# Kernel optimization log

Hardware: AMD Instinct MI355X
Metric: run time of the kernel (lower is better)

The kernel has to match this reference:

```python
import jax, jax.numpy as jnp
import numpy as np

NUDGE = 1e-7

def _norm(x):
    # global mean + L2-norm over axes (1,2), per sample (faithful to source)
    size = x.shape[1] * x.shape[2]
    mean = jnp.sum(x, axis=(1, 2), keepdims=True) / size
    xc = x - mean
    l2 = jnp.sqrt(jnp.sum(xc * xc, axis=(1, 2), keepdims=True))
    return xc / (l2 + NUDGE)


def setup_inputs() -> dict:
    key = jax.random.key(0)
    ks = jax.random.split(key, 9)
    B, D, S, F = 8, 512, 4096, 2048
    s = 0.02
    x = jax.random.normal(ks[0], (B, D, S), dtype=jnp.float32)
    Wq = jax.random.normal(ks[1], (D, D), dtype=jnp.float32) * s
    Wk = jax.random.normal(ks[2], (D, D), dtype=jnp.float32) * s
    Wv = jax.random.normal(ks[3], (D, D), dtype=jnp.float32) * s
    Wo = jax.random.normal(ks[4], (D, D), dtype=jnp.float32) * s
    W1 = jax.random.normal(ks[5], (D, F), dtype=jnp.float32) * s
    b1 = jnp.zeros((F,), dtype=jnp.float32)
    W2 = jax.random.normal(ks[6], (F, D), dtype=jnp.float32) * s
    b2 = jnp.zeros((D,), dtype=jnp.float32)
    return {"x": x, "Wq": Wq, "Wk": Wk, "Wv": Wv, "Wo": Wo,
            "W1": W1, "b1": b1, "W2": W2, "b2": b2}


def reference(x, Wq, Wk, Wv, Wo, W1, b1, W2, b2):
    B, D, S = x.shape
    xt = jnp.swapaxes(x, 1, 2)                      # [B,S,D]
    q = xt @ Wq                                     # [B,S,D]
    k = xt @ Wk
    v = xt @ Wv
    scores = jnp.einsum('bsd,btd->bst', q, k) / jnp.sqrt(jnp.float32(D))
    attn = jax.nn.softmax(scores, axis=-1)          # [B,S,S]
    attn_out = jnp.swapaxes((attn @ v) @ Wo, 1, 2)  # [B,D,S]

    post = _norm(x + attn_out)                      # [B,D,S]

    # per-slice feedforward+linear loop == batched matmul over token axis
    pt = jnp.swapaxes(post, 1, 2)                   # [B,S,D]
    h = jax.nn.relu(pt @ W1 + b1) @ W2 + b2         # [B,S,D]
    return _norm(post + jnp.swapaxes(h, 1, 2))
```

## Files before the change

### kernel.cpp

```cpp
#include <hip/hip_runtime.h>


typedef unsigned short u16;
typedef __attribute__((ext_vector_type(4))) float f32x4;
typedef __attribute__((ext_vector_type(8))) short s16x8;

__device__ __forceinline__ float bf2f(u16 u) {
    unsigned int v = ((unsigned int)u) << 16;
    float f;
    __builtin_memcpy(&f, &v, 4);
    return f;
}
__device__ __forceinline__ u16 f2bf(float f) {
    unsigned int v;
    __builtin_memcpy(&v, &f, 4);
    unsigned int r = (v + 0x7fffu + ((v >> 16) & 1u)) >> 16;
    return (u16)r;
}
__device__ __forceinline__ u16 loadbf(const void* p, long long i, int f32) {
    return f32 ? f2bf(((const float*)p)[i]) : ((const u16*)p)[i];
}

#if defined(__has_builtin)
#if __has_builtin(__builtin_amdgcn_global_load_lds)
#define HAS_GLDS 1
#endif
#endif
#ifndef HAS_GLDS
#define HAS_GLDS 0
#endif

#if HAS_GLDS
__device__ __forceinline__ void glds16(const u16* g, u16* l) {
    __builtin_amdgcn_global_load_lds(
        (const __attribute__((address_space(1))) void*)g,
        (__attribute__((address_space(3))) void*)l, 16, 0, 0);
}
#endif

__global__ __launch_bounds__(256) void detect_f32(
    const u16* __restrict__ p, int n_u16, int* __restrict__ flag)
{
    int insane = 0;
    for (int i = threadIdx.x; i < n_u16; i += 256) {
        u16 h = p[i];
        int e = (h >> 7) & 0xFF;
        int m = h & 0x7F;
        bool sane = (e >= 96 && e <= 141) || (e == 0 && m == 0);
        insane += sane ? 0 : 1;
    }
#pragma unroll
    for (int off = 32; off > 0; off >>= 1) insane += __shfl_down(insane, off);
    __shared__ int red[4];
    if ((threadIdx.x & 63) == 0) red[threadIdx.x >> 6] = insane;
    __syncthreads();
    if (threadIdx.x == 0)
        *flag = (red[0] + red[1] + red[2] + red[3] > n_u16 / 4) ? 1 : 0;
}

#define BM 128
#define BN 128
#define BK 32

template <typename OutT, bool BIAS, bool RELU, bool EXPSUM, bool RDIV>
__global__ __launch_bounds__(256) void gemm_bt(
    const u16* __restrict__ A, const u16* __restrict__ Bt, OutT* __restrict__ C,
    const u16* __restrict__ bias, int M, int N, int K,
    int lda, int ldb, int ldc, int wmod,
    long long aZ, long long aW, long long bZ, long long bW, long long cZ,
    int swz, float* rs, long long rsZ)
{
    __shared__ u16 As[2][BM * BK];
    __shared__ u16 Bs[2][BN * BK];

    const int z = blockIdx.z;
    const int g = z / wmod, w = z - g * wmod;
    A  += g * aZ + w * aW;
    Bt += g * bZ + w * bW;
    C  += (long long)z * cZ;
    if (EXPSUM || RDIV) rs += z * rsZ;

    int bx = blockIdx.x, by = blockIdx.y;
    if (swz) {
        const int gx = gridDim.x;
        int id = by * gx + bx;
        int xcd = id & 7, j = id >> 3;
        bx = j % gx;
        by = (j / gx) * 8 + xcd;
    }

    const int tid = threadIdx.x;
    const int wave = tid >> 6, lane = tid & 63;
    const int wm = wave >> 1, wn = wave & 1;
    const int q = lane >> 4, r = lane & 15;

    const int ar = tid >> 2;
    const int ac = (((tid & 3) ^ ((tid >> 3) & 3)) << 3);
    const int ks = (r >> 1) & 3;

    const u16* Ag = A + (long long)(by * BM + ar) * lda + ac;
    const u16* Bg = Bt + (long long)(bx * BN + ar) * ldb + ac;
    const long long rstepA = 64LL * lda, rstepB = 64LL * ldb;

    f32x4 acc[4][4];
    const f32x4 zero = {0.f, 0.f, 0.f, 0.f};
#pragma unroll
    for (int i = 0; i < 4; ++i)
#pragma unroll
        for (int j = 0; j < 4; ++j) acc[i][j] = zero;

    const int nIter = K / BK;
#if HAS_GLDS
    glds16(Ag, &As[0][tid * 8]);
    glds16(Ag + rstepA, &As[0][2048 + tid * 8]);
    glds16(Bg, &Bs[0][tid * 8]);
    glds16(Bg + rstepB, &Bs[0][2048 + tid * 8]);
    Ag += BK; Bg += BK;
    __syncthreads();
    for (int it = 0; it < nIter; ++it) {
        const int cur = it & 1, nxt = cur ^ 1;
        if (it + 1 < nIter) {
            glds16(Ag, &As[nxt][tid * 8]);
            glds16(Ag + rstepA, &As[nxt][2048 + tid * 8]);
            glds16(Bg, &Bs[nxt][tid * 8]);
            glds16(Bg + rstepB, &Bs[nxt][2048 + tid * 8]);
            Ag += BK; Bg += BK;
        }
        s16x8 af[4], bf[4];
#pragma unroll
        for (int mi = 0; mi < 4; ++mi)
            af[mi] = *(const s16x8*)(&As[cur][(wm * 64 + mi * 16 + r) * BK + ((q ^ ks) << 3)]);
#pragma unroll
        for (int ni = 0; ni < 4; ++ni)
            bf[ni] = *(const s16x8*)(&Bs[cur][(wn * 64 + ni * 16 + r) * BK + ((q ^ ks) << 3)]);
#pragma unroll
        for (int mi = 0; mi < 4; ++mi)
#pragma unroll
            for (int ni = 0; ni < 4; ++ni)
                acc[mi][ni] = __builtin_amdgcn_mfma_f32_16x16x32_bf16(
                    af[mi], bf[ni], acc[mi][ni], 0, 0, 0);
        __syncthreads();
    }
#else
    for (int it = 0; it < nIter; ++it) {
        int4 a0 = *(const int4*)(Ag);
        int4 a1 = *(const int4*)(Ag + rstepA);
        int4 b0 = *(const int4*)(Bg);
        int4 b1 = *(const int4*)(Bg + rstepB);
        Ag += BK; Bg += BK;
        __syncthreads();
        *(int4*)(&As[0][tid * 8]) = a0;
        *(int4*)(&As[0][2048 + tid * 8]) = a1;
        *(int4*)(&Bs[0][tid * 8]) = b0;
        *(int4*)(&Bs[0][2048 + tid * 8]) = b1;
        __syncthreads();
        s16x8 af[4], bf[4];
#pragma unroll
        for (int mi = 0; mi < 4; ++mi)
            af[mi] = *(const s16x8*)(&As[0][(wm * 64 + mi * 16 + r) * BK + ((q ^ ks) << 3)]);
#pragma unroll
        for (int ni = 0; ni < 4; ++ni)
            bf[ni] = *(const s16x8*)(&Bs[0][(wn * 64 + ni * 16 + r) * BK + ((q ^ ks) << 3)]);
#pragma unroll
        for (int mi = 0; mi < 4; ++mi)
#pragma unroll
            for (int ni = 0; ni < 4; ++ni)
                acc[mi][ni] = __builtin_amdgcn_mfma_f32_16x16x32_bf16(
                    af[mi], bf[ni], acc[mi][ni], 0, 0, 0);
    }
#endif

    const int col0 = bx * BN + wn * 64;
    const int row0 = by * BM + wm * 64;
    if constexpr (EXPSUM) {
        const float scale = 0.044194173824159216f;
#pragma unroll
        for (int mi = 0; mi < 4; ++mi) {
#pragma unroll
            for (int rr = 0; rr < 4; ++rr) {
                const int rowg = row0 + mi * 16 + q * 4 + rr;
                float rsum = 0.f;
#pragma unroll
                for (int ni = 0; ni < 4; ++ni) {
                    float v = __expf(fminf(acc[mi][ni][rr] * scale, 30.f));
                    rsum += v;
                    C[(long long)rowg * ldc + col0 + ni * 16 + r] = (OutT)f2bf(v);
                }
#pragma unroll
                for (int o = 1; o < 16; o <<= 1) rsum += __shfl_xor(rsum, o);
                if (r == 0) atomicAdd(&rs[rowg], rsum);
            }
        }
    } else {
#pragma unroll
        for (int ni = 0; ni < 4; ++ni) {
            const int colg = col0 + ni * 16 + r;
            float bv = 0.f;
            if constexpr (BIAS) bv = bf2f(bias[colg]);
#pragma unroll
            for (int mi = 0; mi < 4; ++mi) {
#pragma unroll
                for (int rr = 0; rr < 4; ++rr) {
                    const int rowg = row0 + mi * 16 + q * 4 + rr;
                    float v = acc[mi][ni][rr] + bv;
                    if constexpr (RELU) v = fmaxf(v, 0.f);
                    if constexpr (RDIV) v /= rs[rowg];
                    if constexpr (sizeof(OutT) == 2)
                        C[(long long)rowg * ldc + colg] = (OutT)f2bf(v);
                    else
                        C[(long long)rowg * ldc + colg] = (OutT)v;
                }
            }
        }
    }
}

__global__ __launch_bounds__(256) void transpose_any(
    const void* __restrict__ in, u16* __restrict__ out, int R, int C,
    long long sIn, long long sOut, const int* __restrict__ flag)
{
    __shared__ u16 tile[32][33];
    const int f32 = *flag;
    const long long ib = (long long)blockIdx.z * sIn;
    u16* ob = out + (long long)blockIdx.z * sOut;
    const int c0 = blockIdx.x * 32, r0 = blockIdx.y * 32;
    const int tx = threadIdx.x, ty = threadIdx.y;
#pragma unroll
    for (int i = 0; i < 4; ++i) {
        int rr = ty + i * 8;
        tile[rr][tx] = loadbf(in, ib + (long long)(r0 + rr) * C + c0 + tx, f32);
    }
    __syncthreads();
#pragma unroll
    for (int i = 0; i < 4; ++i) {
        int cc = ty + i * 8;
        ob[(long long)(c0 + cc) * R + r0 + tx] = tile[tx][cc];
    }
}

__global__ __launch_bounds__(256) void transpose_b16(
    const u16* __restrict__ in, u16* __restrict__ out, int R, int C,
    long long sIn, long long sOut)
{
    __shared__ u16 tile[32][33];
    in += (long long)blockIdx.z * sIn;
    out += (long long)blockIdx.z * sOut;
    const int c0 = blockIdx.x * 32, r0 = blockIdx.y * 32;
    const int tx = threadIdx.x, ty = threadIdx.y;
#pragma unroll
    for (int i = 0; i < 4; ++i) {
        int rr = ty + i * 8;
        tile[rr][tx] = in[(long long)(r0 + rr) * C + c0 + tx];
    }
    __syncthreads();
#pragma unroll
    for (int i = 0; i < 4; ++i) {
        int cc = ty + i * 8;
        out[(long long)(c0 + cc) * R + r0 + tx] = tile[tx][cc];
    }
}

__global__ __launch_bounds__(256) void convert_bias(
    const void* __restrict__ b1, const void* __restrict__ b2,
    u16* __restrict__ ob, const int* __restrict__ f1, const int* __restrict__ f2)
{
    int i = blockIdx.x * 256 + threadIdx.x;
    if (i < 2048) ob[i] = loadbf(b1, i, *f1);
    else if (i < 2560) ob[i] = loadbf(b2, i - 2048, *f2);
}

__global__ __launch_bounds__(256) void reduce_legs(
    const float* __restrict__ P, u16* __restrict__ O, int legs,
    const float* __restrict__ l)
{
    const long long SD = 4096LL * 512;
    const int g = blockIdx.y;
    const float* Pg = P + (long long)g * legs * SD;
    const float* lg = l + (long long)g * 4096;
    u16* Og = O + (long long)g * SD;
    const int base = blockIdx.x * 2048;
#pragma unroll
    for (int it = 0; it < 8; ++it) {
        int i = base + it * 256 + threadIdx.x;
        float s = 0.f;
        for (int lj = 0; lj < legs; ++lj) s += Pg[(long long)lj * SD + i];
        Og[i] = f2bf(s / lg[i >> 9]);
    }
}

__global__ __launch_bounds__(256) void stats_add_partial(
    const u16* __restrict__ A, const u16* __restrict__ Bv,
    float2* __restrict__ partial)
{
    const int b = blockIdx.y;
    const long long yb = (long long)b * (4096LL * 512);
    const int base = blockIdx.x * 2048;
    float s = 0.f, ss = 0.f;
#pragma unroll
    for (int it = 0; it < 8; ++it) {
        int i = base + it * 256 + threadIdx.x;
        float z = bf2f(A[yb + i]) + bf2f(Bv[yb + i]);
        s += z; ss += z * z;
    }
#pragma unroll
    for (int off = 32; off > 0; off >>= 1) {
        s += __shfl_down(s, off); ss += __shfl_down(ss, off);
    }
    __shared__ float red[8];
    int lane = threadIdx.x & 63, wave = threadIdx.x >> 6;
    if (lane == 0) { red[wave * 2] = s; red[wave * 2 + 1] = ss; }
    __syncthreads();
    if (threadIdx.x == 0) {
        for (int w = 1; w < 4; ++w) { s += red[w * 2]; ss += red[w * 2 + 1]; }
        partial[b * 1024 + blockIdx.x] = make_float2(s, ss);
    }
}

__global__ __launch_bounds__(256) void stats_finish(
    const float2* __restrict__ partial, float2* __restrict__ stats, float N)
{
    const int b = blockIdx.x;
    float s = 0.f, ss = 0.f;
    for (int i = threadIdx.x; i < 1024; i += 256) {
        float2 p = partial[b * 1024 + i];
        s += p.x; ss += p.y;
    }
#pragma unroll
    for (int off = 32; off > 0; off >>= 1) {
        s += __shfl_down(s, off); ss += __shfl_down(ss, off);
    }
    __shared__ float red[8];
    int lane = threadIdx.x & 63, wave = threadIdx.x >> 6;
    if (lane == 0) { red[wave * 2] = s; red[wave * 2 + 1] = ss; }
    __syncthreads();
    if (threadIdx.x == 0) {
        for (int w = 1; w < 4; ++w) { s += red[w * 2]; ss += red[w * 2 + 1]; }
        float mean = s / N;
        float l2 = sqrtf(fmaxf(ss - s * s / N, 0.f));
        stats[b] = make_float2(mean, 1.f / (l2 + 1e-7f));
    }
}

__global__ __launch_bounds__(256) void post_kernel(
    const u16* __restrict__ A, const u16* __restrict__ Bv,
    const float2* __restrict__ stats, u16* __restrict__ post)
{
    const int b = blockIdx.y;
    const float2 st = stats[b];
    const long long yb = (long long)b * (4096LL * 512);
    const int base = blockIdx.x * 2048;
#pragma unroll
    for (int it = 0; it < 8; ++it) {
        int i = base + it * 256 + threadIdx.x;
        float z = bf2f(A[yb + i]) + bf2f(Bv[yb + i]);
        post[yb + i] = f2bf((z - st.x) * st.y);
    }
}

__global__ __launch_bounds__(256) void final_kernel(
    const u16* __restrict__ P, const u16* __restrict__ G,
    const float2* __restrict__ stats, float* __restrict__ out)
{
    __shared__ float tile[32][33];
    const int b = blockIdx.z;
    const float2 st = stats[b];
    const long long bb = (long long)b * (4096LL * 512);
    const int s0 = blockIdx.x * 32, d0 = blockIdx.y * 32;
    const int tx = threadIdx.x, ty = threadIdx.y;
#pragma unroll
    for (int i = 0; i < 4; ++i) {
        int sl = ty + i * 8;
        long long idx = bb + (long long)(s0 + sl) * 512 + d0 + tx;
        tile[sl][tx] = bf2f(P[idx]) + bf2f(G[idx]);
    }
    __syncthreads();
#pragma unroll
    for (int i = 0; i < 4; ++i) {
        int dl = ty + i * 8;
        out[bb + (long long)(d0 + dl) * 4096 + s0 + tx] =
            (tile[tx][dl] - st.x) * st.y;
    }
}

extern "C" void kernel_launch(void* const* d_in, const int* in_sizes, int n_in,
                              void* d_out, int out_size, void* d_ws, size_t ws_size,
                              hipStream_t stream)
{
    (void)out_size;
    const void* x  = d_in[0];
    const void* Wq = d_in[1];
    const void* Wk = d_in[2];
    const void* Wv = d_in[3];
    const void* Wo = d_in[4];
    const void* W1 = d_in[5];
    const void* b1 = d_in[6];
    const void* W2 = d_in[7];
    const void* b2 = d_in[8];

    const int Bb = 8, D = 512, S = 4096, F = 2048;
    const long long SD = (long long)S * D;
    const long long DD = (long long)D * D;
    const long long SS = (long long)S * S;

    char* ws = (char*)d_ws;
    size_t off = 0;
    auto take = [&](size_t bytes) -> char* {
        char* p = ws + off;
        off += (bytes + 255) & ~(size_t)255;
        return p;
    };
    u16* xt   = (u16*)take((size_t)Bb * SD * 2);
    u16* WqT  = (u16*)take((size_t)DD * 2);
    u16* WkT  = (u16*)take((size_t)DD * 2);
    u16* WvT  = (u16*)take((size_t)DD * 2);
    u16* WoT  = (u16*)take((size_t)DD * 2);
    u16* W1T  = (u16*)take((size_t)D * F * 2);
    u16* W2T  = (u16*)take((size_t)D * F * 2);
    u16* bb   = (u16*)take(2560 * 2);
    u16* post = (u16*)take((size_t)Bb * SD * 2);
    float2* npart  = (float2*)take(8 * 1024 * sizeof(float2));
    float2* stats1v = (float2*)take(256);
    float2* stats2v = (float2*)take(256);
    int* flags = (int*)take(16 * sizeof(int));
    float* rowsums = (float*)take((size_t)Bb * S * sizeof(float));

    size_t remaining = ws_size > off ? ws_size - off : 0;
    const size_t perG = (size_t)4 * SD * 2 + (size_t)SS * 2 + 65536;
    int G = (remaining >= 8 * perG) ? 8 : (remaining >= 4 * perG) ? 4
          : (remaining >= 2 * perG) ? 2 : 1;
    int legs = (G == 1) ? 4 : (G == 2) ? 2 : 1;

    u16* QKV    = (u16*)take((size_t)3 * G * SD * 2);
    u16* Vt     = (u16*)take((size_t)G * SD * 2);
    u16* scores = (u16*)take((size_t)G * SS * 2);
    float* partK = (float*)post;
    u16* Oall = (u16*)d_out;
    u16* Y    = scores;
    u16* Hbuf = (u16*)d_out;
    u16* Gbuf = scores;

    for (int i = 0; i < 9 && i < n_in; ++i) {
        int n = in_sizes[i] < 8192 ? in_sizes[i] : 8192;
        detect_f32<<<1, 256, 0, stream>>>((const u16*)d_in[i], n, flags + i);
    }

    dim3 tb(32, 8, 1);
    transpose_any<<<dim3(S / 32, D / 32, Bb), tb, 0, stream>>>(x, xt, D, S, SD, SD, flags + 0);
    transpose_any<<<dim3(16, 16, 1), tb, 0, stream>>>(Wq, WqT, D, D, 0, 0, flags + 1);
    transpose_any<<<dim3(16, 16, 1), tb, 0, stream>>>(Wk, WkT, D, D, 0, 0, flags + 2);
    transpose_any<<<dim3(16, 16, 1), tb, 0, stream>>>(Wv, WvT, D, D, 0, 0, flags + 3);
    transpose_any<<<dim3(16, 16, 1), tb, 0, stream>>>(Wo, WoT, D, D, 0, 0, flags + 4);
    transpose_any<<<dim3(F / 32, D / 32, 1), tb, 0, stream>>>(W1, W1T, D, F, 0, 0, flags + 5);
    transpose_any<<<dim3(D / 32, F / 32, 1), tb, 0, stream>>>(W2, W2T, F, D, 0, 0, flags + 7);
    convert_bias<<<10, 256, 0, stream>>>(b1, b2, bb, flags + 6, flags + 8);
    hipMemsetAsync(rowsums, 0, (size_t)Bb * S * sizeof(float), stream);

    for (int b0 = 0; b0 < Bb; b0 += G) {
        gemm_bt<u16, false, false, false, false><<<dim3(D / 128, S / 128, 3 * G), 256, 0, stream>>>(
            xt + (long long)b0 * SD, WqT, QKV, nullptr, S, D, D, D, D, D,
            3, SD, 0, 0, DD, SD, 1, nullptr, 0);
        transpose_b16<<<dim3(D / 32, S / 32, G), tb, 0, stream>>>(
            QKV + 2 * SD, Vt, S, D, 3 * SD, SD);
        gemm_bt<u16, false, false, true, false><<<dim3(S / 128, S / 128, G), 256, 0, stream>>>(
            QKV, QKV + SD, scores, nullptr, S, S, D, D, D, S,
            1, 3 * SD, 0, 3 * SD, 0, SS, 1, rowsums + (long long)b0 * S, S);
        if (legs == 1) {
            gemm_bt<u16, false, false, false, true><<<dim3(D / 128, S / 128, G), 256, 0, stream>>>(
                scores, Vt, Oall + (long long)b0 * SD, nullptr, S, D, S, S, S, D,
                1, SS, 0, SD, 0, SD, 1, rowsums + (long long)b0 * S, S);
        } else {
            gemm_bt<float, false, false, false, false><<<dim3(D / 128, S / 128, G * legs), 256, 0, stream>>>(
                scores, Vt, partK, nullptr, S, D, S / legs, S, S, D,
                legs, SS, S / legs, SD, S / legs, SD, 1, nullptr, 0);
            reduce_legs<<<dim3(1024, G), 256, 0, stream>>>(
                partK, Oall + (long long)b0 * SD, legs, rowsums + (long long)b0 * S);
        }
    }

    gemm_bt<u16, false, false, false, false><<<dim3(D / 128, (Bb * S) / 128, 1), 256, 0, stream>>>(
        Oall, WoT, Y, nullptr, Bb * S, D, D, D, D, D, 1, 0, 0, 0, 0, 0, 1, nullptr, 0);

    stats_add_partial<<<dim3(1024, Bb), 256, 0, stream>>>(xt, Y, npart);
    stats_finish<<<dim3(Bb), 256, 0, stream>>>(npart, stats1v, (float)SD);
    post_kernel<<<dim3(1024, Bb), 256, 0, stream>>>(xt, Y, stats1v, post);

    for (int h = 0; h < 2; ++h) {
        gemm_bt<u16, true, true, false, false><<<dim3(F / 128, (4 * S) / 128, 1), 256, 0, stream>>>(
            post + (long long)h * 4 * SD, W1T, Hbuf, bb, 4 * S, F, D, D, D, F,
            1, 0, 0, 0, 0, 0, 1, nullptr, 0);
        gemm_bt<u16, true, false, false, false><<<dim3(D / 128, (4 * S) / 128, 1), 256, 0, stream>>>(
            Hbuf, W2T, Gbuf + (long long)h * 4 * SD, bb + 2048, 4 * S, D, F, F, F, D,
            1, 0, 0, 0, 0, 0, 1, nullptr, 0);
    }

    stats_add_partial<<<dim3(1024, Bb), 256, 0, stream>>>(post, Gbuf, npart);
    stats_finish<<<dim3(Bb), 256, 0, stream>>>(npart, stats2v, (float)SD);
    final_kernel<<<dim3(S / 32, D / 32, Bb), tb, 0, stream>>>(
        post, Gbuf, stats2v, (float*)d_out);
}
```

Before: 1.148 ms.

## Fuse attention into flash-style kernel and batch input dtype detection

Replaces the separate QK^T exp-score GEMM plus PV GEMM, which wrote a full SxS score matrix to memory, with a fused flash-attention kernel. It keeps Q tiles in LDS, streams K tiles, forms exp-probabilities in LDS and accumulates P·V in registers, then normalizes by the row sums. The max-free exp with clamp is kept, and an optional split-K path with a reduction kernel remains for small workspaces. The nine per-input detect launches are merged into one kernel. The new kernel uses large LDS and 512 threads, so occupancy is low, and V is read directly from global memory without staging.

```diff
diff --git a/kernel.cpp b/kernel.cpp
--- a/kernel.cpp
+++ b/kernel.cpp
@@ -36,11 +36,18 @@
         (const __attribute__((address_space(1))) void*)g,
         (__attribute__((address_space(3))) void*)l, 16, 0, 0);
 }
+#else
+__device__ __forceinline__ void glds16(const u16* g, u16* l) {
+    *(int4*)l = *(const int4*)g;
+}
 #endif
 
-__global__ __launch_bounds__(256) void detect_f32(
-    const u16* __restrict__ p, int n_u16, int* __restrict__ flag)
-{
+struct DetectArgs { const u16* p[9]; int n[9]; };
+
+__global__ __launch_bounds__(256) void detect9(DetectArgs a, int* __restrict__ flags)
+{
+    const u16* p = a.p[blockIdx.x];
+    const int n_u16 = a.n[blockIdx.x];
     int insane = 0;
     for (int i = threadIdx.x; i < n_u16; i += 256) {
         u16 h = p[i];
@@ -55,20 +62,20 @@
     if ((threadIdx.x & 63) == 0) red[threadIdx.x >> 6] = insane;
     __syncthreads();
     if (threadIdx.x == 0)
-        *flag = (red[0] + red[1] + red[2] + red[3] > n_u16 / 4) ? 1 : 0;
+        flags[blockIdx.x] = (red[0] + red[1] + red[2] + red[3] > n_u16 / 4) ? 1 : 0;
 }
 
 #define BM 128
 #define BN 128
 #define BK 32
 
-template <typename OutT, bool BIAS, bool RELU, bool EXPSUM, bool RDIV>
+template <typename OutT, bool BIAS, bool RELU>
 __global__ __launch_bounds__(256) void gemm_bt(
     const u16* __restrict__ A, const u16* __restrict__ Bt, OutT* __restrict__ C,
     const u16* __restrict__ bias, int M, int N, int K,
     int lda, int ldb, int ldc, int wmod,
     long long aZ, long long aW, long long bZ, long long bW, long long cZ,
-    int swz, float* rs, long long rsZ)
+    int swz)
 {
     __shared__ u16 As[2][BM * BK];
     __shared__ u16 Bs[2][BN * BK];
@@ -78,7 +85,6 @@
     A  += g * aZ + w * aW;
     Bt += g * bZ + w * bW;
     C  += (long long)z * cZ;
-    if (EXPSUM || RDIV) rs += z * rsZ;
 
     int bx = blockIdx.x, by = blockIdx.y;
     if (swz) {
@@ -110,7 +116,6 @@
         for (int j = 0; j < 4; ++j) acc[i][j] = zero;
 
     const int nIter = K / BK;
-#if HAS_GLDS
     glds16(Ag, &As[0][tid * 8]);
     glds16(Ag + rstepA, &As[0][2048 + tid * 8]);
     glds16(Bg, &Bs[0][tid * 8]);
@@ -141,77 +146,239 @@
                     af[mi], bf[ni], acc[mi][ni], 0, 0, 0);
         __syncthreads();
     }
-#else
-    for (int it = 0; it < nIter; ++it) {
-        int4 a0 = *(const int4*)(Ag);
-        int4 a1 = *(const int4*)(Ag + rstepA);
-        int4 b0 = *(const int4*)(Bg);
-        int4 b1 = *(const int4*)(Bg + rstepB);
-        Ag += BK; Bg += BK;
-        __syncthreads();
-        *(int4*)(&As[0][tid * 8]) = a0;
-        *(int4*)(&As[0][2048 + tid * 8]) = a1;
-        *(int4*)(&Bs[0][tid * 8]) = b0;
-        *(int4*)(&Bs[0][2048 + tid * 8]) = b1;
-        __syncthreads();
-        s16x8 af[4], bf[4];
-#pragma unroll
-        for (int mi = 0; mi < 4; ++mi)
-            af[mi] = *(const s16x8*)(&As[0][(wm * 64 + mi * 16 + r) * BK + ((q ^ ks) << 3)]);
-#pragma unroll
-        for (int ni = 0; ni < 4; ++ni)
-            bf[ni] = *(const s16x8*)(&Bs[0][(wn * 64 + ni * 16 + r) * BK + ((q ^ ks) << 3)]);
-#pragma unroll
-        for (int mi = 0; mi < 4; ++mi)
-#pragma unroll
-            for (int ni = 0; ni < 4; ++ni)
-                acc[mi][ni] = __builtin_amdgcn_mfma_f32_16x16x32_bf16(
-                    af[mi], bf[ni], acc[mi][ni], 0, 0, 0);
-    }
-#endif
 
     const int col0 = bx * BN + wn * 64;
     const int row0 = by * BM + wm * 64;
-    if constexpr (EXPSUM) {
-        const float scale = 0.044194173824159216f;
+#pragma unroll
+    for (int ni = 0; ni < 4; ++ni) {
+        const int colg = col0 + ni * 16 + r;
+        float bv = 0.f;
+        if constexpr (BIAS) bv = bf2f(bias[colg]);
 #pragma unroll
         for (int mi = 0; mi < 4; ++mi) {
 #pragma unroll
             for (int rr = 0; rr < 4; ++rr) {
                 const int rowg = row0 + mi * 16 + q * 4 + rr;
-                float rsum = 0.f;
-#pragma unroll
-                for (int ni = 0; ni < 4; ++ni) {
-                    float v = __expf(fminf(acc[mi][ni][rr] * scale, 30.f));
-                    rsum += v;
-                    C[(long long)rowg * ldc + col0 + ni * 16 + r] = (OutT)f2bf(v);
+                float v = acc[mi][ni][rr] + bv;
+                if constexpr (RELU) v = fmaxf(v, 0.f);
+                if constexpr (sizeof(OutT) == 2)
+                    C[(long long)rowg * ldc + colg] = (OutT)f2bf(v);
+                else
+                    C[(long long)rowg * ldc + colg] = (OutT)v;
+            }
+        }
+    }
+}
+
+template <bool DIRECT>
+__global__ __launch_bounds__(512, 2) void flash_attn(
+    const u16* __restrict__ QKV,
+    const u16* __restrict__ Vt,
+    u16* __restrict__ O,
+    float* __restrict__ Opart,
+    float* __restrict__ rsPart,
+    int nsplit)
+{
+    __shared__ u16 Qs[64 * 512];
+    __shared__ u16 Ks[2][128 * 128];
+    __shared__ u16 Ps[64 * 136];
+    __shared__ float rsL[8][64];
+
+    const long long SD = 4096LL * 512;
+    const int g = blockIdx.z, sp = blockIdx.y;
+    const int q0 = blockIdx.x * 64;
+    const u16* Qg = QKV + ((long long)g * 3 + 0) * SD;
+    const u16* Kg = QKV + ((long long)g * 3 + 1) * SD;
+    const u16* Vg = Vt + (long long)g * SD;
+
+    const int tid = threadIdx.x;
+    const int wave = tid >> 6, lane = tid & 63;
+    const int q = lane >> 4, r = lane & 15;
+    const int mg = wave >> 2, ng = wave & 3;
+    const int dg = wave;
+
+#pragma unroll
+    for (int i = 0; i < 8; ++i) {
+        int L = i * 512 + tid;
+        int row = L >> 6, p = L & 63;
+        int l = p ^ (row & 15);
+        glds16(Qg + (long long)(q0 + row) * 512 + l * 8, &Qs[L * 8]);
+    }
+
+    f32x4 oacc[4][4];
+    const f32x4 zero = {0.f, 0.f, 0.f, 0.f};
+#pragma unroll
+    for (int i = 0; i < 4; ++i)
+#pragma unroll
+        for (int j = 0; j < 4; ++j) oacc[i][j] = zero;
+    float rsum[2][4] = {{0.f, 0.f, 0.f, 0.f}, {0.f, 0.f, 0.f, 0.f}};
+
+    const int span = 4096 / nsplit;
+    const int kt0 = sp * span;
+    const int ktN = span / 128;
+    const float scale = 0.044194173824159216f;
+
+    auto stageK = [&](int ktile, int kc, int buf) {
+#pragma unroll
+        for (int i = 0; i < 4; ++i) {
+            int L = i * 512 + tid;
+            int row = L >> 4, p = L & 15;
+            int l = p ^ (row & 15);
+            glds16(Kg + (long long)(kt0 + ktile * 128 + row) * 512 + kc * 128 + l * 8,
+                   &Ks[buf][L * 8]);
+        }
+    };
+    stageK(0, 0, 0);
+
+    for (int kt = 0; kt < ktN; ++kt) {
+        f32x4 sacc[2][2];
+#pragma unroll
+        for (int i = 0; i < 2; ++i)
+#pragma unroll
+            for (int j = 0; j < 2; ++j) sacc[i][j] = zero;
+
+        for (int kc = 0; kc < 4; ++kc) {
+            if (kc < 3) stageK(kt, kc + 1, (kc + 1) & 1);
+            __syncthreads();
+            const u16* Kb = Ks[kc & 1];
+#pragma unroll
+            for (int sc = 0; sc < 4; ++sc) {
+                s16x8 af[2], bf[2];
+#pragma unroll
+                for (int mi = 0; mi < 2; ++mi) {
+                    int row = (mg * 2 + mi) * 16 + r;
+                    int l = kc * 16 + sc * 4 + q;
+                    af[mi] = *(const s16x8*)&Qs[row * 512 + ((l ^ r) << 3)];
                 }
 #pragma unroll
-                for (int o = 1; o < 16; o <<= 1) rsum += __shfl_xor(rsum, o);
-                if (r == 0) atomicAdd(&rs[rowg], rsum);
+                for (int ni = 0; ni < 2; ++ni) {
+                    int row = (ng * 2 + ni) * 16 + r;
+                    int l = sc * 4 + q;
+                    bf[ni] = *(const s16x8*)&Kb[row * 128 + ((l ^ r) << 3)];
+                }
+#pragma unroll
+                for (int mi = 0; mi < 2; ++mi)
+#pragma unroll
+                    for (int ni = 0; ni < 2; ++ni)
+                        sacc[mi][ni] = __builtin_amdgcn_mfma_f32_16x16x32_bf16(
+                            af[mi], bf[ni], sacc[mi][ni], 0, 0, 0);
             }
         }
-    } else {
-#pragma unroll
-        for (int ni = 0; ni < 4; ++ni) {
-            const int colg = col0 + ni * 16 + r;
-            float bv = 0.f;
-            if constexpr (BIAS) bv = bf2f(bias[colg]);
-#pragma unroll
-            for (int mi = 0; mi < 4; ++mi) {
+#pragma unroll
+        for (int mi = 0; mi < 2; ++mi) {
+#pragma unroll
+            for (int ni = 0; ni < 2; ++ni) {
+                int col = (ng * 2 + ni) * 16 + r;
 #pragma unroll
                 for (int rr = 0; rr < 4; ++rr) {
-                    const int rowg = row0 + mi * 16 + q * 4 + rr;
-                    float v = acc[mi][ni][rr] + bv;
-                    if constexpr (RELU) v = fmaxf(v, 0.f);
-                    if constexpr (RDIV) v /= rs[rowg];
-                    if constexpr (sizeof(OutT) == 2)
-                        C[(long long)rowg * ldc + colg] = (OutT)f2bf(v);
-                    else
-                        C[(long long)rowg * ldc + colg] = (OutT)v;
+                    int row = (mg * 2 + mi) * 16 + q * 4 + rr;
+                    float v = __expf(fminf(sacc[mi][ni][rr] * scale, 30.f));
+                    Ps[row * 136 + col] = f2bf(v);
+                    rsum[mi][rr] += v;
                 }
             }
         }
+        if (kt + 1 < ktN) stageK(kt + 1, 0, 0);
+        __syncthreads();
+        const long long vbase = (long long)(dg * 64 + r) * 4096 + kt0 + kt * 128;
+#pragma unroll
+        for (int kc = 0; kc < 4; ++kc) {
+            s16x8 af[4], bf[4];
+#pragma unroll
+            for (int mi = 0; mi < 4; ++mi)
+                af[mi] = *(const s16x8*)(Vg + vbase + (long long)mi * 16 * 4096
+                                         + kc * 32 + q * 8);
+#pragma unroll
+            for (int ni = 0; ni < 4; ++ni)
+                bf[ni] = *(const s16x8*)&Ps[(ni * 16 + r) * 136 + kc * 32 + q * 8];
+#pragma unroll
+            for (int mi = 0; mi < 4; ++mi)
+#pragma unroll
+                for (int ni = 0; ni < 4; ++ni)
+                    oacc[mi][ni] = __builtin_amdgcn_mfma_f32_16x16x32_bf16(
+                        af[mi], bf[ni], oacc[mi][ni], 0, 0, 0);
+        }
+    }
+
+#pragma unroll
+    for (int mi = 0; mi < 2; ++mi)
+#pragma unroll
+        for (int rr = 0; rr < 4; ++rr) {
+            float s = rsum[mi][rr];
+#pragma unroll
+            for (int m = 1; m < 16; m <<= 1) s += __shfl_xor(s, m);
+            rsum[mi][rr] = s;
+        }
+    if (r == 0) {
+#pragma unroll
+        for (int mi = 0; mi < 2; ++mi)
+#pragma unroll
+            for (int rr = 0; rr < 4; ++rr)
+                rsL[wave][(mg * 2 + mi) * 16 + q * 4 + rr] = rsum[mi][rr];
+    }
+    __syncthreads();
+
+    if constexpr (DIRECT) {
+        u16* Og = O + (long long)g * SD;
+#pragma unroll
+        for (int ni = 0; ni < 4; ++ni) {
+            int qrow = ni * 16 + r;
+            int wb = (qrow >> 5) * 4;
+            float rs = rsL[wb][qrow] + rsL[wb + 1][qrow]
+                     + rsL[wb + 2][qrow] + rsL[wb + 3][qrow];
+            float inv = 1.f / rs;
+#pragma unroll
+            for (int mi = 0; mi < 4; ++mi) {
+                int d = (dg * 4 + mi) * 16 + q * 4;
+                ushort4 o4;
+                o4.x = f2bf(oacc[mi][ni][0] * inv);
+                o4.y = f2bf(oacc[mi][ni][1] * inv);
+                o4.z = f2bf(oacc[mi][ni][2] * inv);
+                o4.w = f2bf(oacc[mi][ni][3] * inv);
+                *(ushort4*)&Og[(long long)(q0 + qrow) * 512 + d] = o4;
+            }
+        }
+    } else {
+        const int pb = g * nsplit + sp;
+        float* Op = Opart + (long long)pb * SD;
+#pragma unroll
+        for (int ni = 0; ni < 4; ++ni) {
+            int qrow = ni * 16 + r;
+#pragma unroll
+            for (int mi = 0; mi < 4; ++mi) {
+                int d = (dg * 4 + mi) * 16 + q * 4;
+                float4 o4;
+                o4.x = oacc[mi][ni][0]; o4.y = oacc[mi][ni][1];
+                o4.z = oacc[mi][ni][2]; o4.w = oacc[mi][ni][3];
+                *(float4*)&Op[(long long)(q0 + qrow) * 512 + d] = o4;
+            }
+        }
+        if (tid < 64) {
+            int wb = (tid >> 5) * 4;
+            rsPart[(long long)pb * 4096 + q0 + tid] =
+                rsL[wb][tid] + rsL[wb + 1][tid] + rsL[wb + 2][tid] + rsL[wb + 3][tid];
+        }
+    }
+}
+
+__global__ __launch_bounds__(256) void reduce_flash(
+    const float* __restrict__ Opart, const float* __restrict__ rsPart,
+    u16* __restrict__ O, int ns)
+{
+    const long long SD = 4096LL * 512;
+    const int g = blockIdx.y;
+    u16* Og = O + (long long)g * SD;
+    const int base = blockIdx.x * 2048;
+#pragma unroll
+    for (int it = 0; it < 8; ++it) {
+        int i = base + it * 256 + threadIdx.x;
+        int row = i >> 9;
+        float s = 0.f, rs = 0.f;
+        for (int sp = 0; sp < ns; ++sp) {
+            s += Opart[(long long)(g * ns + sp) * SD + i];
+            rs += rsPart[(long long)(g * ns + sp) * 4096 + row];
+        }
+        Og[i] = f2bf(s / rs);
     }
 }
 
@@ -267,25 +434,6 @@
     int i = blockIdx.x * 256 + threadIdx.x;
     if (i < 2048) ob[i] = loadbf(b1, i, *f1);
     else if (i < 2560) ob[i] = loadbf(b2, i - 2048, *f2);
-}
-
-__global__ __launch_bounds__(256) void reduce_legs(
-    const float* __restrict__ P, u16* __restrict__ O, int legs,
-    const float* __restrict__ l)
-{
-    const long long SD = 4096LL * 512;
-    const int g = blockIdx.y;
-    const float* Pg = P + (long long)g * legs * SD;
-    const float* lg = l + (long long)g * 4096;
-    u16* Og = O + (long long)g * SD;
-    const int base = blockIdx.x * 2048;
-#pragma unroll
-    for (int it = 0; it < 8; ++it) {
-        int i = base + it * 256 + threadIdx.x;
-        float s = 0.f;
-        for (int lj = 0; lj < legs; ++lj) s += Pg[(long long)lj * SD + i];
-        Og[i] = f2bf(s / lg[i >> 9]);
-    }
 }
 
 __global__ __launch_bounds__(256) void stats_add_partial(
@@ -400,7 +548,6 @@
     const int Bb = 8, D = 512, S = 4096, F = 2048;
     const long long SD = (long long)S * D;
     const long long DD = (long long)D * D;
-    const long long SS = (long long)S * S;
 
     char* ws = (char*)d_ws;
     size_t off = 0;
@@ -422,27 +569,28 @@
     float2* stats1v = (float2*)take(256);
     float2* stats2v = (float2*)take(256);
     int* flags = (int*)take(16 * sizeof(int));
-    float* rowsums = (float*)take((size_t)Bb * S * sizeof(float));
+    float* rsPart = (float*)take(4 * 4096 * sizeof(float));
 
     size_t remaining = ws_size > off ? ws_size - off : 0;
-    const size_t perG = (size_t)4 * SD * 2 + (size_t)SS * 2 + 65536;
-    int G = (remaining >= 8 * perG) ? 8 : (remaining >= 4 * perG) ? 4
-          : (remaining >= 2 * perG) ? 2 : 1;
-    int legs = (G == 1) ? 4 : (G == 2) ? 2 : 1;
-
-    u16* QKV    = (u16*)take((size_t)3 * G * SD * 2);
-    u16* Vt     = (u16*)take((size_t)G * SD * 2);
-    u16* scores = (u16*)take((size_t)G * SS * 2);
-    float* partK = (float*)post;
+    const size_t perG = (size_t)4 * SD * 2 + 4096;
+    int G = (remaining >= 8 * perG) ? 8 : (remaining >= 4 * perG) ? 4 : 2;
+    int ns = (G >= 4) ? 1 : 2;
+
+    u16* attnBuf = (u16*)take((size_t)4 * G * SD * 2);
+    u16* QKVb = attnBuf;
+    u16* Vtb  = attnBuf + (size_t)3 * G * SD;
+    float* Opart = (float*)post;
     u16* Oall = (u16*)d_out;
-    u16* Y    = scores;
+    u16* Y    = post;
     u16* Hbuf = (u16*)d_out;
-    u16* Gbuf = scores;
-
-    for (int i = 0; i < 9 && i < n_in; ++i) {
-        int n = in_sizes[i] < 8192 ? in_sizes[i] : 8192;
-        detect_f32<<<1, 256, 0, stream>>>((const u16*)d_in[i], n, flags + i);
-    }
+    u16* Gbuf = attnBuf;
+
+    DetectArgs da;
+    for (int i = 0; i < 9; ++i) {
+        da.p[i] = (const u16*)d_in[i];
+        da.n[i] = (i < n_in && in_sizes[i] < 8192) ? in_sizes[i] : 8192;
+    }
+    detect9<<<dim3(9), 256, 0, stream>>>(da, flags);
 
     dim3 tb(32, 8, 1);
     transpose_any<<<dim3(S / 32, D / 32, Bb), tb, 0, stream>>>(x, xt, D, S, SD, SD, flags + 0);
@@ -453,44 +601,38 @@
     transpose_any<<<dim3(F / 32, D / 32, 1), tb, 0, stream>>>(W1, W1T, D, F, 0, 0, flags + 5);
     transpose_any<<<dim3(D / 32, F / 32, 1), tb, 0, stream>>>(W2, W2T, F, D, 0, 0, flags + 7);
     convert_bias<<<10, 256, 0, stream>>>(b1, b2, bb, flags + 6, flags + 8);
-    hipMemsetAsync(rowsums, 0, (size_t)Bb * S * sizeof(float), stream);
 
     for (int b0 = 0; b0 < Bb; b0 += G) {
-        gemm_bt<u16, false, false, false, false><<<dim3(D / 128, S / 128, 3 * G), 256, 0, stream>>>(
-            xt + (long long)b0 * SD, WqT, QKV, nullptr, S, D, D, D, D, D,
-            3, SD, 0, 0, DD, SD, 1, nullptr, 0);
+        gemm_bt<u16, false, false><<<dim3(D / 128, S / 128, 3 * G), 256, 0, stream>>>(
+            xt + (long long)b0 * SD, WqT, QKVb, nullptr, S, D, D, D, D, D,
+            3, SD, 0, 0, DD, SD, 1);
         transpose_b16<<<dim3(D / 32, S / 32, G), tb, 0, stream>>>(
-            QKV + 2 * SD, Vt, S, D, 3 * SD, SD);
-        gemm_bt<u16, false, false, true, false><<<dim3(S / 128, S / 128, G), 256, 0, stream>>>(
-            QKV, QKV + SD, scores, nullptr, S, S, D, D, D, S,
-            1, 3 * SD, 0, 3 * SD, 0, SS, 1, rowsums + (long long)b0 * S, S);
-        if (legs == 1) {
-            gemm_bt<u16, false, false, false, true><<<dim3(D / 128, S / 128, G), 256, 0, stream>>>(
-                scores, Vt, Oall + (long long)b0 * SD, nullptr, S, D, S, S, S, D,
-                1, SS, 0, SD, 0, SD, 1, rowsums + (long long)b0 * S, S);
+            QKVb + 2 * SD, Vtb, S, D, 3 * SD, SD);
+        if (ns == 1) {
+            flash_attn<true><<<dim3(64, 1, G), 512, 0, stream>>>(
+                QKVb, Vtb, Oall + (long long)b0 * SD, nullptr, nullptr, 1);
         } else {
-            gemm_bt<float, false, false, false, false><<<dim3(D / 128, S / 128, G * legs), 256, 0, stream>>>(
-                scores, Vt, partK, nullptr, S, D, S / legs, S, S, D,
-                legs, SS, S / legs, SD, S / legs, SD, 1, nullptr, 0);
-            reduce_legs<<<dim3(1024, G), 256, 0, stream>>>(
-                partK, Oall + (long long)b0 * SD, legs, rowsums + (long long)b0 * S);
-        }
-    }
-
-    gemm_bt<u16, false, false, false, false><<<dim3(D / 128, (Bb * S) / 128, 1), 256, 0, stream>>>(
-        Oall, WoT, Y, nullptr, Bb * S, D, D, D, D, D, 1, 0, 0, 0, 0, 0, 1, nullptr, 0);
+            flash_attn<false><<<dim3(64, ns, G), 512, 0, stream>>>(
+                QKVb, Vtb, nullptr, Opart, rsPart, ns);
+            reduce_flash<<<dim3(1024, G), 256, 0, stream>>>(
+                Opart, rsPart, Oall + (long long)b0 * SD, ns);
+        }
+    }
+
+    gemm_bt<u16, false, false><<<dim3(D / 128, (Bb * S) / 128, 1), 256, 0, stream>>>(
+        Oall, WoT, Y, nullptr, Bb * S, D, D, D, D, D, 1, 0, 0, 0, 0, 0, 1);
 
     stats_add_partial<<<dim3(1024, Bb), 256, 0, stream>>>(xt, Y, npart);
     stats_finish<<<dim3(Bb), 256, 0, stream>>>(npart, stats1v, (float)SD);
     post_kernel<<<dim3(1024, Bb), 256, 0, stream>>>(xt, Y, stats1v, post);
 
     for (int h = 0; h < 2; ++h) {
-        gemm_bt<u16, true, true, false, false><<<dim3(F / 128, (4 * S) / 128, 1), 256, 0, stream>>>(
+        gemm_bt<u16, true, true><<<dim3(F / 128, (4 * S) / 128, 1), 256, 0, stream>>>(
             post + (long long)h * 4 * SD, W1T, Hbuf, bb, 4 * S, F, D, D, D, F,
-            1, 0, 0, 0, 0, 0, 1, nullptr, 0);
-        gemm_bt<u16, true, false, false, false><<<dim3(D / 128, (4 * S) / 128, 1), 256, 0, stream>>>(
+            1, 0, 0, 0, 0, 0, 1);
+        gemm_bt<u16, true, false><<<dim3(D / 128, (4 * S) / 128, 1), 256, 0, stream>>>(
             Hbuf, W2T, Gbuf + (long long)h * 4 * SD, bb + 2048, 4 * S, D, F, F, F, D,
-            1, 0, 0, 0, 0, 0, 1, nullptr, 0);
+            1, 0, 0, 0, 0, 0, 1);
     }
 
     stats_add_partial<<<dim3(1024, Bb), 256, 0, stream>>>(post, Gbuf, npart);
```

Result: faster. 1.021 ms (-11.0%).
